# Optimization experiments

Hardware: AMD Instinct MI355X
Metric: run time of the kernel (lower is better)

## Reference

```python
import jax, jax.numpy as jnp
import numpy as np

TOP_K = 2
TEMP = 1.0

def setup_inputs() -> dict:
    key = jax.random.key(0)
    ks = jax.random.split(key, 7)
    B, T, D, E = 2, 2048, 768, 8
    F = 4 * D
    s = 0.02
    return {
        "x": jax.random.normal(ks[0], (B, T, D), dtype=jnp.float32),
        "gate_w": jax.random.normal(ks[1], (D, E), dtype=jnp.float32) * s,
        "gate_b": jnp.zeros((E,), dtype=jnp.float32),
        "w1": jax.random.normal(ks[2], (E, D, F), dtype=jnp.float32) * s,
        "b1": jnp.zeros((E, F), dtype=jnp.float32),
        "w2": jax.random.normal(ks[3], (E, F, D), dtype=jnp.float32) * s,
        "b2": jnp.zeros((E, D), dtype=jnp.float32),
    }

def reference(x, gate_w, gate_b, w1, b1, w2, b2):
    B, T, D = x.shape
    E = gate_w.shape[1]
    x_flat = x.reshape(-1, D)                       # [N, D]
    logits = x_flat @ gate_w + gate_b              # [N, E]
    gates = jax.nn.softmax(logits / TEMP, axis=-1)
    topk_gates, topk_idx = jax.lax.top_k(gates, TOP_K)   # [N, K]
    topk_gates = topk_gates / (jnp.sum(topk_gates, axis=-1, keepdims=True) + 1e-9)
    # Dense combine weights: w[n, e] = sum_k topk_gates[n, k] * (topk_idx[n, k] == e)
    combine = jnp.sum(
        topk_gates[:, :, None] * jax.nn.one_hot(topk_idx, E, dtype=x.dtype),
        axis=1,
    )                                               # [N, E]
    out = jnp.zeros_like(x_flat)
    for e in range(E):  # fixed small expert loop (structurally distinct params)
        h = jax.nn.gelu(x_flat @ w1[e] + b1[e], approximate=False)  # [N, 4D]
        y = h @ w2[e] + b2[e]                                       # [N, D]
        out = out + combine[:, e:e + 1] * y
    return out.reshape(B, T, D)
```

## Files before the change

### kernel.cpp

```cpp
#include <hip/hip_runtime.h>
#include <hip/hip_bf16.h>


#define N_TOK 4096
#define DIM   768
#define FDIM  3072
#define NEXP  8

typedef __attribute__((ext_vector_type(8))) _Float16 f16x8;
typedef __attribute__((ext_vector_type(4))) _Float16 f16x4;
typedef __attribute__((ext_vector_type(4))) float     f32x4;

__device__ __forceinline__ float gelu_fast(float v) {
    float u = 0.7978845608f * v * (1.0f + 0.044715f * v * v);
    float t = 1.0f - 2.0f / (1.0f + __expf(2.0f * u));
    return 0.5f * v * (1.0f + t);
}

__global__ __launch_bounds__(256) void cast_x_kernel(const float* __restrict__ x,
                                                     _Float16* __restrict__ xh) {
    int i = blockIdx.x * 256 + threadIdx.x;
    float4 v = ((const float4*)x)[i];
    f16x4 o;
    o[0] = (_Float16)v.x; o[1] = (_Float16)v.y;
    o[2] = (_Float16)v.z; o[3] = (_Float16)v.w;
    ((f16x4*)xh)[i] = o;
}

__global__ __launch_bounds__(256) void transpose_cast_kernel(const float* __restrict__ in,
                                                             _Float16* __restrict__ out,
                                                             int R, int C) {
    const int e  = blockIdx.z;
    const size_t eoff = (size_t)e * R * C;
    const int c0 = blockIdx.x * 64;
    const int r0 = blockIdx.y * 64;
    __shared__ _Float16 tile[64][66];
    const int t = threadIdx.x;
    #pragma unroll
    for (int it = 0; it < 4; it++) {
        int lin = it * 256 + t;
        int r  = lin >> 4;
        int c4 = lin & 15;
        float4 v = *(const float4*)&in[eoff + (size_t)(r0 + r) * C + c0 + c4 * 4];
        tile[r][c4 * 4 + 0] = (_Float16)v.x;
        tile[r][c4 * 4 + 1] = (_Float16)v.y;
        tile[r][c4 * 4 + 2] = (_Float16)v.z;
        tile[r][c4 * 4 + 3] = (_Float16)v.w;
    }
    __syncthreads();
    #pragma unroll
    for (int it = 0; it < 4; it++) {
        int lin = it * 256 + t;
        int c  = lin >> 4;
        int r4 = lin & 15;
        f16x4 o;
        #pragma unroll
        for (int j = 0; j < 4; j++) o[j] = tile[r4 * 4 + j][c];
        *(f16x4*)&out[eoff + (size_t)(c0 + c) * R + r0 + r4 * 4] = o;
    }
}

__global__ __launch_bounds__(256) void gate_kernel(const float* __restrict__ x,
                                                   const float* __restrict__ gw,
                                                   const float* __restrict__ gb,
                                                   int* __restrict__ tok_list,
                                                   float* __restrict__ wt_list,
                                                   int* __restrict__ count,
                                                   int2* __restrict__ inv) {
    const int gtid = blockIdx.x * 256 + threadIdx.x;
    const int n    = gtid >> 6;
    const int lane = threadIdx.x & 63;
    if (n >= N_TOK) return;
    double part[NEXP];
    #pragma unroll
    for (int e = 0; e < NEXP; e++) part[e] = 0.0;
    for (int d = lane; d < DIM; d += 64) {
        float xv = x[n * DIM + d];
        const float* g = &gw[d * NEXP];
        #pragma unroll
        for (int e = 0; e < NEXP; e++) part[e] += (double)xv * (double)g[e];
    }
    #pragma unroll
    for (int e = 0; e < NEXP; e++) {
        double v = part[e];
        #pragma unroll
        for (int off = 32; off > 0; off >>= 1) v += __shfl_xor(v, off);
        part[e] = v + (double)gb[e];
    }
    if (lane == 0) {
        double mx = part[0];
        #pragma unroll
        for (int e = 1; e < NEXP; e++) mx = fmax(mx, part[e]);
        double ex[NEXP]; double s = 0.0;
        #pragma unroll
        for (int e = 0; e < NEXP; e++) { ex[e] = exp(part[e] - mx); s += ex[e]; }
        int i0 = 0;
        #pragma unroll
        for (int e = 1; e < NEXP; e++) if (ex[e] > ex[i0]) i0 = e;
        int i1 = (i0 == 0) ? 1 : 0;
        #pragma unroll
        for (int e = 0; e < NEXP; e++) if (e != i0 && ex[e] > ex[i1]) i1 = e;
        float g0 = (float)(ex[i0] / s), g1 = (float)(ex[i1] / s);
        float dn = g0 + g1 + 1e-9f;
        float w0 = g0 / dn, w1 = g1 / dn;
        int s0 = atomicAdd(&count[i0], 1);
        tok_list[i0 * N_TOK + s0] = n;  wt_list[i0 * N_TOK + s0] = w0;
        int s1 = atomicAdd(&count[i1], 1);
        tok_list[i1 * N_TOK + s1] = n;  wt_list[i1 * N_TOK + s1] = w1;
        inv[n] = make_int2((i0 << 16) | s0, (i1 << 16) | s1);
    }
}

__global__ void scan_kernel(const int* __restrict__ count, int* __restrict__ basep) {
    if (threadIdx.x == 0) {
        int s = 0;
        for (int e = 0; e < NEXP; e++) { basep[e] = s; s += count[e]; }
    }
}

__global__ __launch_bounds__(256) void mm1_kernel(const _Float16* __restrict__ xh,
                                                  const _Float16* __restrict__ w1t,
                                                  const float* __restrict__ bias1,
                                                  const int* __restrict__ tok_list,
                                                  const int* __restrict__ count,
                                                  const int* __restrict__ basep,
                                                  _Float16* __restrict__ h) {
    const int e    = blockIdx.z;
    const int cnt  = count[e];
    const int row0 = blockIdx.y * 128;
    if (row0 >= cnt) return;
    const int col0 = blockIdx.x * 128;
    const int t    = threadIdx.x;
    const int lane = t & 63;
    const int wv   = t >> 6;
    const int wy   = wv >> 1, wx = wv & 1;
    const int m_lane = lane & 15, quad = lane >> 4;

    __shared__ __align__(16) _Float16 smem[128 * 132];
    _Float16* As = smem;
    _Float16* Bs = smem + 4096;

    const int b0 = wv * 2, b1 = b0 + 1;
    int ra0 = row0 + b0 * 16 + m_lane; if (ra0 > cnt - 1) ra0 = cnt - 1;
    int ra1 = row0 + b1 * 16 + m_lane; if (ra1 > cnt - 1) ra1 = cnt - 1;
    const int tokA0 = tok_list[e * N_TOK + ra0];
    const int tokA1 = tok_list[e * N_TOK + ra1];
    const _Float16* pa0 = xh + (size_t)tokA0 * DIM + quad * 8;
    const _Float16* pa1 = xh + (size_t)tokA1 * DIM + quad * 8;
    const _Float16* pb0 = w1t + (size_t)e * FDIM * DIM
                        + (size_t)(col0 + b0 * 16 + m_lane) * DIM + quad * 8;
    const _Float16* pb1 = pb0 + (size_t)16 * DIM;

    f32x4 acc[4][4];
    #pragma unroll
    for (int i = 0; i < 4; i++)
        #pragma unroll
        for (int j = 0; j < 4; j++)
            acc[i][j] = (f32x4){0.f, 0.f, 0.f, 0.f};

    const int NK = DIM / 32;
    uint4 rA0 = *(const uint4*)pa0;
    uint4 rA1 = *(const uint4*)pa1;
    uint4 rB0 = *(const uint4*)pb0;
    uint4 rB1 = *(const uint4*)pb1;

    for (int k = 0; k < NK; k++) {
        __syncthreads();
        *(uint4*)&As[b0 * 512 + lane * 8] = rA0;
        *(uint4*)&As[b1 * 512 + lane * 8] = rA1;
        *(uint4*)&Bs[b0 * 512 + lane * 8] = rB0;
        *(uint4*)&Bs[b1 * 512 + lane * 8] = rB1;
        if (k + 1 < NK) {
            const int off = (k + 1) * 32;
            rA0 = *(const uint4*)(pa0 + off);
            rA1 = *(const uint4*)(pa1 + off);
            rB0 = *(const uint4*)(pb0 + off);
            rB1 = *(const uint4*)(pb1 + off);
        }
        __syncthreads();
        f16x8 af[4], bf[4];
        #pragma unroll
        for (int i = 0; i < 4; i++)
            af[i] = *(const f16x8*)&As[(wy * 4 + i) * 512 + lane * 8];
        #pragma unroll
        for (int j = 0; j < 4; j++)
            bf[j] = *(const f16x8*)&Bs[(wx * 4 + j) * 512 + lane * 8];
        #pragma unroll
        for (int i = 0; i < 4; i++)
            #pragma unroll
            for (int j = 0; j < 4; j++)
                acc[i][j] = __builtin_amdgcn_mfma_f32_16x16x32_f16(af[i], bf[j], acc[i][j], 0, 0, 0);
    }

    __syncthreads();
    float bj[4];
    #pragma unroll
    for (int j = 0; j < 4; j++)
        bj[j] = bias1[e * FDIM + col0 + wx * 64 + j * 16 + m_lane];
    #pragma unroll
    for (int i = 0; i < 4; i++)
        #pragma unroll
        for (int j = 0; j < 4; j++)
            #pragma unroll
            for (int r = 0; r < 4; r++) {
                int rr = wy * 64 + i * 16 + quad * 4 + r;
                int cc = wx * 64 + j * 16 + m_lane;
                smem[rr * 132 + cc] = (_Float16)gelu_fast(acc[i][j][r] + bj[j]);
            }
    __syncthreads();
    const int hbase = basep[e];
    #pragma unroll
    for (int s = 0; s < 8; s++) {
        int chunk = s * 256 + t;
        int row = chunk >> 4;
        int col = (chunk & 15) * 8;
        if (row0 + row < cnt) {
            f16x4 lo = *(const f16x4*)&smem[row * 132 + col];
            f16x4 hi = *(const f16x4*)&smem[row * 132 + col + 4];
            f16x8 v;
            v[0]=lo[0]; v[1]=lo[1]; v[2]=lo[2]; v[3]=lo[3];
            v[4]=hi[0]; v[5]=hi[1]; v[6]=hi[2]; v[7]=hi[3];
            *(f16x8*)&h[(size_t)(hbase + row0 + row) * FDIM + col0 + col] = v;
        }
    }
}

__global__ __launch_bounds__(256) void mm2_kernel(const _Float16* __restrict__ h,
                                                  const _Float16* __restrict__ w2t,
                                                  const float* __restrict__ bias2,
                                                  const float* __restrict__ wt_list,
                                                  const int* __restrict__ count,
                                                  const int* __restrict__ basep,
                                                  _Float16* __restrict__ y) {
    const int e    = blockIdx.z;
    const int cnt  = count[e];
    const int row0 = blockIdx.y * 128;
    if (row0 >= cnt) return;
    const int col0 = blockIdx.x * 128;
    const int t    = threadIdx.x;
    const int lane = t & 63;
    const int wv   = t >> 6;
    const int wy   = wv >> 1, wx = wv & 1;
    const int m_lane = lane & 15, quad = lane >> 4;

    __shared__ __align__(16) _Float16 smem[128 * 132];
    _Float16* As = smem;
    _Float16* Bs = smem + 4096;

    const int hbase = basep[e];
    const int b0 = wv * 2, b1 = b0 + 1;
    int ra0 = row0 + b0 * 16 + m_lane; if (ra0 > cnt - 1) ra0 = cnt - 1;
    int ra1 = row0 + b1 * 16 + m_lane; if (ra1 > cnt - 1) ra1 = cnt - 1;
    const _Float16* pa0 = h + (size_t)(hbase + ra0) * FDIM + quad * 8;
    const _Float16* pa1 = h + (size_t)(hbase + ra1) * FDIM + quad * 8;
    const _Float16* pb0 = w2t + (size_t)e * DIM * FDIM
                        + (size_t)(col0 + b0 * 16 + m_lane) * FDIM + quad * 8;
    const _Float16* pb1 = pb0 + (size_t)16 * FDIM;

    f32x4 acc[4][4];
    #pragma unroll
    for (int i = 0; i < 4; i++)
        #pragma unroll
        for (int j = 0; j < 4; j++)
            acc[i][j] = (f32x4){0.f, 0.f, 0.f, 0.f};

    const int NK = FDIM / 32;
    uint4 rA0 = *(const uint4*)pa0;
    uint4 rA1 = *(const uint4*)pa1;
    uint4 rB0 = *(const uint4*)pb0;
    uint4 rB1 = *(const uint4*)pb1;

    for (int k = 0; k < NK; k++) {
        __syncthreads();
        *(uint4*)&As[b0 * 512 + lane * 8] = rA0;
        *(uint4*)&As[b1 * 512 + lane * 8] = rA1;
        *(uint4*)&Bs[b0 * 512 + lane * 8] = rB0;
        *(uint4*)&Bs[b1 * 512 + lane * 8] = rB1;
        if (k + 1 < NK) {
            const int off = (k + 1) * 32;
            rA0 = *(const uint4*)(pa0 + off);
            rA1 = *(const uint4*)(pa1 + off);
            rB0 = *(const uint4*)(pb0 + off);
            rB1 = *(const uint4*)(pb1 + off);
        }
        __syncthreads();
        f16x8 af[4], bf[4];
        #pragma unroll
        for (int i = 0; i < 4; i++)
            af[i] = *(const f16x8*)&As[(wy * 4 + i) * 512 + lane * 8];
        #pragma unroll
        for (int j = 0; j < 4; j++)
            bf[j] = *(const f16x8*)&Bs[(wx * 4 + j) * 512 + lane * 8];
        #pragma unroll
        for (int i = 0; i < 4; i++)
            #pragma unroll
            for (int j = 0; j < 4; j++)
                acc[i][j] = __builtin_amdgcn_mfma_f32_16x16x32_f16(af[i], bf[j], acc[i][j], 0, 0, 0);
    }

    __syncthreads();
    float bj[4];
    #pragma unroll
    for (int j = 0; j < 4; j++)
        bj[j] = bias2[e * DIM + col0 + wx * 64 + j * 16 + m_lane];
    #pragma unroll
    for (int i = 0; i < 4; i++) {
        #pragma unroll
        for (int r = 0; r < 4; r++) {
            int rr = wy * 64 + i * 16 + quad * 4 + r;
            float wgt = wt_list[e * N_TOK + row0 + rr];
            #pragma unroll
            for (int j = 0; j < 4; j++) {
                int cc = wx * 64 + j * 16 + m_lane;
                smem[rr * 132 + cc] = (_Float16)(wgt * (acc[i][j][r] + bj[j]));
            }
        }
    }
    __syncthreads();
    #pragma unroll
    for (int s = 0; s < 8; s++) {
        int chunk = s * 256 + t;
        int row = chunk >> 4;
        int col = (chunk & 15) * 8;
        if (row0 + row < cnt) {
            f16x4 lo = *(const f16x4*)&smem[row * 132 + col];
            f16x4 hi = *(const f16x4*)&smem[row * 132 + col + 4];
            f16x8 v;
            v[0]=lo[0]; v[1]=lo[1]; v[2]=lo[2]; v[3]=lo[3];
            v[4]=hi[0]; v[5]=hi[1]; v[6]=hi[2]; v[7]=hi[3];
            *(f16x8*)&y[(size_t)(hbase + row0 + row) * DIM + col0 + col] = v;
        }
    }
}

__global__ __launch_bounds__(192) void combine_kernel(const _Float16* __restrict__ y,
                                                      const int2* __restrict__ inv,
                                                      const int* __restrict__ basep,
                                                      float* __restrict__ out) {
    const int n = blockIdx.x * 2 + (threadIdx.x >= 96);
    const int c = (threadIdx.x % 96) * 8;
    int2 iv = inv[n];
    int s0 = basep[(iv.x >> 16) & 0x7] + (iv.x & 0xffff);
    int s1 = basep[(iv.y >> 16) & 0x7] + (iv.y & 0xffff);
    f16x8 a = *(const f16x8*)&y[(size_t)s0 * DIM + c];
    f16x8 b = *(const f16x8*)&y[(size_t)s1 * DIM + c];
    float4 o0, o1;
    o0.x = (float)a[0] + (float)b[0];  o0.y = (float)a[1] + (float)b[1];
    o0.z = (float)a[2] + (float)b[2];  o0.w = (float)a[3] + (float)b[3];
    o1.x = (float)a[4] + (float)b[4];  o1.y = (float)a[5] + (float)b[5];
    o1.z = (float)a[6] + (float)b[6];  o1.w = (float)a[7] + (float)b[7];
    *(float4*)&out[(size_t)n * DIM + c]     = o0;
    *(float4*)&out[(size_t)n * DIM + c + 4] = o1;
}

extern "C" void kernel_launch(void* const* d_in, const int* in_sizes, int n_in,
                              void* d_out, int out_size, void* d_ws, size_t ws_size,
                              hipStream_t stream) {
    const float* x  = (const float*)d_in[0];
    const float* gw = (const float*)d_in[1];
    const float* gb = (const float*)d_in[2];
    const float* w1 = (const float*)d_in[3];
    const float* b1 = (const float*)d_in[4];
    const float* w2 = (const float*)d_in[5];
    const float* b2 = (const float*)d_in[6];
    float* out = (float*)d_out;

    char* ws = (char*)d_ws;
    _Float16* xh   = (_Float16*)ws;
    _Float16* w1t  = xh  + (size_t)N_TOK * DIM;
    _Float16* w2t  = w1t + (size_t)NEXP * FDIM * DIM;
    _Float16* hbuf = w2t + (size_t)NEXP * DIM * FDIM;
    int*   tok_list = (int*)(hbuf + (size_t)2 * N_TOK * FDIM);
    float* wt_list  = (float*)(tok_list + NEXP * N_TOK);
    int2*  inv      = (int2*)(wt_list + NEXP * N_TOK);
    int*   count    = (int*)(inv + N_TOK);
    int*   basep    = count + 8;
    _Float16* ybuf  = w1t;

    hipMemsetAsync(count, 0, 64, stream);

    cast_x_kernel<<<dim3(N_TOK * DIM / 4 / 256), 256, 0, stream>>>(x, xh);
    transpose_cast_kernel<<<dim3(FDIM / 64, DIM / 64, NEXP), 256, 0, stream>>>(w1, w1t, DIM, FDIM);
    transpose_cast_kernel<<<dim3(DIM / 64, FDIM / 64, NEXP), 256, 0, stream>>>(w2, w2t, FDIM, DIM);
    gate_kernel<<<dim3(N_TOK / 4), 256, 0, stream>>>(x, gw, gb, tok_list, wt_list, count, inv);
    scan_kernel<<<1, 64, 0, stream>>>(count, basep);
    mm1_kernel<<<dim3(FDIM / 128, N_TOK / 128, NEXP), 256, 0, stream>>>(
        xh, w1t, b1, tok_list, count, basep, hbuf);
    mm2_kernel<<<dim3(DIM / 128, N_TOK / 128, NEXP), 256, 0, stream>>>(
        hbuf, w2t, b2, wt_list, count, basep, ybuf);
    combine_kernel<<<dim3(N_TOK / 2), 192, 0, stream>>>(ybuf, inv, basep, out);
}
```

Before: 540.9 us.

## Split-K mm2 with atomic scatter-add into output, drop combine kernel

Splits the second expert GEMM's K dimension four ways, giving four times as many blocks, and has each block atomically add its weighted partial results straight into the fp32 output rows of the owning tokens. This removes the intermediate fp16 y buffer, the inverse index map and the separate combine kernel. The output is zeroed with a memset first. The cost is many fp32 global atomics and non-deterministic summation order. Intermediate y is no longer rounded to fp16.

```diff
diff --git a/kernel.cpp b/kernel.cpp
--- a/kernel.cpp
+++ b/kernel.cpp
@@ -65,8 +65,7 @@
                                                    const float* __restrict__ gb,
                                                    int* __restrict__ tok_list,
                                                    float* __restrict__ wt_list,
-                                                   int* __restrict__ count,
-                                                   int2* __restrict__ inv) {
+                                                   int* __restrict__ count) {
     const int gtid = blockIdx.x * 256 + threadIdx.x;
     const int n    = gtid >> 6;
     const int lane = threadIdx.x & 63;
@@ -107,7 +106,6 @@
         tok_list[i0 * N_TOK + s0] = n;  wt_list[i0 * N_TOK + s0] = w0;
         int s1 = atomicAdd(&count[i1], 1);
         tok_list[i1 * N_TOK + s1] = n;  wt_list[i1 * N_TOK + s1] = w1;
-        inv[n] = make_int2((i0 << 16) | s0, (i1 << 16) | s1);
     }
 }
 
@@ -228,33 +226,35 @@
 __global__ __launch_bounds__(256) void mm2_kernel(const _Float16* __restrict__ h,
                                                   const _Float16* __restrict__ w2t,
                                                   const float* __restrict__ bias2,
+                                                  const int* __restrict__ tok_list,
                                                   const float* __restrict__ wt_list,
                                                   const int* __restrict__ count,
                                                   const int* __restrict__ basep,
-                                                  _Float16* __restrict__ y) {
-    const int e    = blockIdx.z;
+                                                  float* __restrict__ out) {
+    const int e    = blockIdx.z >> 2;
+    const int kp   = blockIdx.z & 3;
     const int cnt  = count[e];
     const int row0 = blockIdx.y * 128;
     if (row0 >= cnt) return;
     const int col0 = blockIdx.x * 128;
+    const int kbase = kp * (FDIM / 4);
     const int t    = threadIdx.x;
     const int lane = t & 63;
     const int wv   = t >> 6;
     const int wy   = wv >> 1, wx = wv & 1;
     const int m_lane = lane & 15, quad = lane >> 4;
 
-    __shared__ __align__(16) _Float16 smem[128 * 132];
-    _Float16* As = smem;
-    _Float16* Bs = smem + 4096;
+    __shared__ __align__(16) _Float16 As[4096];
+    __shared__ __align__(16) _Float16 Bs[4096];
 
     const int hbase = basep[e];
     const int b0 = wv * 2, b1 = b0 + 1;
     int ra0 = row0 + b0 * 16 + m_lane; if (ra0 > cnt - 1) ra0 = cnt - 1;
     int ra1 = row0 + b1 * 16 + m_lane; if (ra1 > cnt - 1) ra1 = cnt - 1;
-    const _Float16* pa0 = h + (size_t)(hbase + ra0) * FDIM + quad * 8;
-    const _Float16* pa1 = h + (size_t)(hbase + ra1) * FDIM + quad * 8;
+    const _Float16* pa0 = h + (size_t)(hbase + ra0) * FDIM + kbase + quad * 8;
+    const _Float16* pa1 = h + (size_t)(hbase + ra1) * FDIM + kbase + quad * 8;
     const _Float16* pb0 = w2t + (size_t)e * DIM * FDIM
-                        + (size_t)(col0 + b0 * 16 + m_lane) * FDIM + quad * 8;
+                        + (size_t)(col0 + b0 * 16 + m_lane) * FDIM + kbase + quad * 8;
     const _Float16* pb1 = pb0 + (size_t)16 * FDIM;
 
     f32x4 acc[4][4];
@@ -264,7 +264,7 @@
         for (int j = 0; j < 4; j++)
             acc[i][j] = (f32x4){0.f, 0.f, 0.f, 0.f};
 
-    const int NK = FDIM / 32;
+    const int NK = (FDIM / 4) / 32;
     uint4 rA0 = *(const uint4*)pa0;
     uint4 rA1 = *(const uint4*)pa1;
     uint4 rB0 = *(const uint4*)pb0;
@@ -298,59 +298,28 @@
                 acc[i][j] = __builtin_amdgcn_mfma_f32_16x16x32_f16(af[i], bf[j], acc[i][j], 0, 0, 0);
     }
 
-    __syncthreads();
     float bj[4];
     #pragma unroll
     for (int j = 0; j < 4; j++)
-        bj[j] = bias2[e * DIM + col0 + wx * 64 + j * 16 + m_lane];
+        bj[j] = (kp == 0) ? bias2[e * DIM + col0 + wx * 64 + j * 16 + m_lane] : 0.0f;
     #pragma unroll
     for (int i = 0; i < 4; i++) {
         #pragma unroll
         for (int r = 0; r < 4; r++) {
-            int rr = wy * 64 + i * 16 + quad * 4 + r;
-            float wgt = wt_list[e * N_TOK + row0 + rr];
-            #pragma unroll
-            for (int j = 0; j < 4; j++) {
-                int cc = wx * 64 + j * 16 + m_lane;
-                smem[rr * 132 + cc] = (_Float16)(wgt * (acc[i][j][r] + bj[j]));
+            int rl = wy * 64 + i * 16 + quad * 4 + r;
+            int gr = row0 + rl;
+            if (gr < cnt) {
+                int tok   = tok_list[e * N_TOK + gr];
+                float wgt = wt_list[e * N_TOK + gr];
+                float* orow = out + (size_t)tok * DIM;
+                #pragma unroll
+                for (int j = 0; j < 4; j++) {
+                    int c = col0 + wx * 64 + j * 16 + m_lane;
+                    atomicAdd(&orow[c], wgt * (acc[i][j][r] + bj[j]));
+                }
             }
         }
     }
-    __syncthreads();
-    #pragma unroll
-    for (int s = 0; s < 8; s++) {
-        int chunk = s * 256 + t;
-        int row = chunk >> 4;
-        int col = (chunk & 15) * 8;
-        if (row0 + row < cnt) {
-            f16x4 lo = *(const f16x4*)&smem[row * 132 + col];
-            f16x4 hi = *(const f16x4*)&smem[row * 132 + col + 4];
-            f16x8 v;
-            v[0]=lo[0]; v[1]=lo[1]; v[2]=lo[2]; v[3]=lo[3];
-            v[4]=hi[0]; v[5]=hi[1]; v[6]=hi[2]; v[7]=hi[3];
-            *(f16x8*)&y[(size_t)(hbase + row0 + row) * DIM + col0 + col] = v;
-        }
-    }
-}
-
-__global__ __launch_bounds__(192) void combine_kernel(const _Float16* __restrict__ y,
-                                                      const int2* __restrict__ inv,
-                                                      const int* __restrict__ basep,
-                                                      float* __restrict__ out) {
-    const int n = blockIdx.x * 2 + (threadIdx.x >= 96);
-    const int c = (threadIdx.x % 96) * 8;
-    int2 iv = inv[n];
-    int s0 = basep[(iv.x >> 16) & 0x7] + (iv.x & 0xffff);
-    int s1 = basep[(iv.y >> 16) & 0x7] + (iv.y & 0xffff);
-    f16x8 a = *(const f16x8*)&y[(size_t)s0 * DIM + c];
-    f16x8 b = *(const f16x8*)&y[(size_t)s1 * DIM + c];
-    float4 o0, o1;
-    o0.x = (float)a[0] + (float)b[0];  o0.y = (float)a[1] + (float)b[1];
-    o0.z = (float)a[2] + (float)b[2];  o0.w = (float)a[3] + (float)b[3];
-    o1.x = (float)a[4] + (float)b[4];  o1.y = (float)a[5] + (float)b[5];
-    o1.z = (float)a[6] + (float)b[6];  o1.w = (float)a[7] + (float)b[7];
-    *(float4*)&out[(size_t)n * DIM + c]     = o0;
-    *(float4*)&out[(size_t)n * DIM + c + 4] = o1;
 }
 
 extern "C" void kernel_launch(void* const* d_in, const int* in_sizes, int n_in,
@@ -372,21 +341,19 @@
     _Float16* hbuf = w2t + (size_t)NEXP * DIM * FDIM;
     int*   tok_list = (int*)(hbuf + (size_t)2 * N_TOK * FDIM);
     float* wt_list  = (float*)(tok_list + NEXP * N_TOK);
-    int2*  inv      = (int2*)(wt_list + NEXP * N_TOK);
-    int*   count    = (int*)(inv + N_TOK);
+    int*   count    = (int*)(wt_list + NEXP * N_TOK);
     int*   basep    = count + 8;
-    _Float16* ybuf  = w1t;
 
     hipMemsetAsync(count, 0, 64, stream);
+    hipMemsetAsync(out, 0, (size_t)out_size * sizeof(float), stream);
 
     cast_x_kernel<<<dim3(N_TOK * DIM / 4 / 256), 256, 0, stream>>>(x, xh);
     transpose_cast_kernel<<<dim3(FDIM / 64, DIM / 64, NEXP), 256, 0, stream>>>(w1, w1t, DIM, FDIM);
     transpose_cast_kernel<<<dim3(DIM / 64, FDIM / 64, NEXP), 256, 0, stream>>>(w2, w2t, FDIM, DIM);
-    gate_kernel<<<dim3(N_TOK / 4), 256, 0, stream>>>(x, gw, gb, tok_list, wt_list, count, inv);
+    gate_kernel<<<dim3(N_TOK / 4), 256, 0, stream>>>(x, gw, gb, tok_list, wt_list, count);
     scan_kernel<<<1, 64, 0, stream>>>(count, basep);
     mm1_kernel<<<dim3(FDIM / 128, N_TOK / 128, NEXP), 256, 0, stream>>>(
         xh, w1t, b1, tok_list, count, basep, hbuf);
-    mm2_kernel<<<dim3(DIM / 128, N_TOK / 128, NEXP), 256, 0, stream>>>(
-        hbuf, w2t, b2, wt_list, count, basep, ybuf);
-    combine_kernel<<<dim3(N_TOK / 2), 192, 0, stream>>>(ybuf, inv, basep, out);
-}
+    mm2_kernel<<<dim3(DIM / 128, N_TOK / 128, NEXP * 4), 256, 0, stream>>>(
+        hbuf, w2t, b2, tok_list, wt_list, count, basep, out);
+}
```

New measurement: 548.8 us. No clear change (+1.5%).
